# Performance work log

Hardware: AMD Instinct MI355X
Metric: run time of the kernel (lower is better)

Reference implementation:

```python
import math
import jax, jax.numpy as jnp
from jax import lax
import numpy as np

SPARSITY = 0.05
EMBEDDING_SIZE = 2048
BATCH = 32768


def setup_inputs() -> dict:
    key = jax.random.key(0)
    k0, k1, k2 = jax.random.split(key, 3)
    x = jax.random.normal(k0, (BATCH, 28, 28), dtype=jnp.float32)
    # conv: out=5, in=1, k=3, no bias (kaiming-ish scale)
    conv_w = jax.random.normal(k1, (5, 1, 3, 3), dtype=jnp.float32) * (1.0 / math.sqrt(9))
    bn_gamma = jnp.ones((5,), jnp.float32)
    bn_beta = jnp.zeros((5,), jnp.float32)
    bn_mean = jnp.zeros((5,), jnp.float32)
    bn_var = jnp.ones((5,), jnp.float32)
    # fc: [EMBEDDING_SIZE, 320], no bias
    fc_w = jax.random.normal(k2, (EMBEDDING_SIZE, 5 * 8 * 8), dtype=jnp.float32) * (1.0 / math.sqrt(320))
    return {"x": x, "conv_w": conv_w, "bn_gamma": bn_gamma, "bn_beta": bn_beta,
            "bn_mean": bn_mean, "bn_var": bn_var, "fc_w": fc_w}


def _kwta(z):
    # k-winners-take-all: top k_active entries per row -> 1, rest -> 0.
    k_active = math.ceil(SPARSITY * z.shape[1])
    topv, _ = lax.top_k(z, k_active)          # [B, k]
    thr = topv[:, -1:]                         # kth largest per row
    binary = (z >= thr).astype(z.dtype)
    # straight-through: forward = binary, backward = identity
    return z + lax.stop_gradient(binary - z)


def reference(x, conv_w, bn_gamma, bn_beta, bn_mean, bn_var, fc_w):
    h = x[:, None, :, :]  # [B,1,28,28]
    h = lax.conv_general_dilated(h, conv_w, window_strides=(1, 1), padding="VALID",
                                 dimension_numbers=("NCHW", "OIHW", "NCHW"))  # [B,5,26,26]
    inv_std = bn_gamma / jnp.sqrt(bn_var + 1e-5)
    h = (h - bn_mean[None, :, None, None]) * inv_std[None, :, None, None] + bn_beta[None, :, None, None]
    h = jnp.maximum(h, 0.0)
    # max_pool2d(kernel=3, stride=3), floor mode -> [B,5,8,8]
    h = lax.reduce_window(h, -jnp.inf, lax.max, (1, 1, 3, 3), (1, 1, 3, 3), "VALID")
    h = h.reshape(h.shape[0], -1)              # [B,320]
    z = h @ fc_w.T                             # [B,EMBEDDING_SIZE]
    return _kwta(z)
```

## Files before the change

### kernel.cpp

```cpp
#include <hip/hip_runtime.h>
#include <math.h>

#define BATCH 32768
#define EMB   2048
#define KDIM  320
#define KACT  103

#define BM 16
#define GTHREADS 512

#define CIMG 16

__global__ __launch_bounds__(256) void transpose_w_kernel(const float* __restrict__ W,
                                                          float* __restrict__ WT) {
  __shared__ float tile[32][33];
  const int k0 = blockIdx.x * 32;
  const int n0 = blockIdx.y * 32;
  const int tx = threadIdx.x;
  const int ty = threadIdx.y;
  for (int i = ty; i < 32; i += 8)
    tile[i][tx] = W[(size_t)(n0 + i) * KDIM + k0 + tx];
  __syncthreads();
  for (int i = ty; i < 32; i += 8)
    WT[(size_t)(k0 + i) * EMB + n0 + tx] = tile[tx][i];
}

__global__ __launch_bounds__(512) void conv_pool_kernel(const float* __restrict__ x,
                                                        const float* __restrict__ cw,
                                                        const float* __restrict__ gamma,
                                                        const float* __restrict__ beta,
                                                        const float* __restrict__ mean,
                                                        const float* __restrict__ var,
                                                        float* __restrict__ Ht) {
#pragma clang fp contract(off)
  __shared__ float xs[CIMG * 784];
  __shared__ float hs[KDIM * 17];
  __shared__ float wv[45];
  __shared__ float inv_s[5], mu_s[5], be_s[5];
  const int t  = threadIdx.x;
  const int b0 = blockIdx.x * CIMG;

  {
    const float4* src = (const float4*)(x + (size_t)b0 * 784);
    float4* dst = (float4*)xs;
    for (int i = t; i < CIMG * 196; i += 512) dst[i] = src[i];
  }
  if (t < 45) wv[t] = cw[t];
  if (t < 5) {
    inv_s[t] = gamma[t] / sqrtf(var[t] + 1e-5f);
    mu_s[t] = mean[t];
    be_s[t] = beta[t];
  }
  __syncthreads();

  const int i0   = t >> 6;
  const int lane = t & 63;
  const int py = lane >> 3;
  const int px = lane & 7;

  for (int ii = 0; ii < 2; ++ii) {
    const int img = i0 * 2 + ii;
    const float* xb = xs + img * 784;

    float xr[5][5];
#pragma unroll
    for (int i = 0; i < 5; ++i)
#pragma unroll
      for (int j = 0; j < 5; ++j)
        xr[i][j] = xb[(3 * py + i) * 28 + 3 * px + j];

#pragma unroll
    for (int c = 0; c < 5; ++c) {
      float wr[9];
#pragma unroll
      for (int i = 0; i < 9; ++i) wr[i] = wv[c * 9 + i];
      const float inv = inv_s[c], mu = mu_s[c], be = be_s[c];
      float mx = -__builtin_huge_valf();
#pragma unroll
      for (int ry = 0; ry < 3; ++ry)
#pragma unroll
        for (int rx = 0; rx < 3; ++rx) {
          float s = 0.0f;
#pragma unroll
          for (int di = 0; di < 3; ++di)
#pragma unroll
            for (int dj = 0; dj < 3; ++dj)
              s = __builtin_fmaf(xr[ry + di][rx + dj], wr[di * 3 + dj], s);
          float t1 = s - mu;
          float t2 = t1 * inv;
          float t3 = t2 + be;
          mx = fmaxf(mx, t3);
        }
      hs[(c * 64 + lane) * 17 + img] = fmaxf(mx, 0.0f);
    }
  }
  __syncthreads();

  for (int idx = t; idx < KDIM * CIMG; idx += 512) {
    const int k = idx >> 4;
    const int img = idx & 15;
    Ht[(size_t)k * BATCH + b0 + img] = hs[k * 17 + img];
  }
}

__global__ __launch_bounds__(GTHREADS) void gemm_topk_kernel(const float* __restrict__ Ht,
                                                             const float* __restrict__ WT,
                                                             float* __restrict__ out) {
  __shared__ unsigned histo[BM * 256];
  __shared__ unsigned prefix_s[BM];
  __shared__ unsigned rank_s[BM];

  const int t    = threadIdx.x;
  const int lane = t & 63;
  const int w    = t >> 6;
  const int m0   = blockIdx.x * BM;
  const int nt   = t * 4;

  if (t < BM) { prefix_s[t] = 0u; rank_s[t] = KACT; }

  float acc[BM][4];
#pragma unroll
  for (int m = 0; m < BM; ++m)
#pragma unroll
    for (int j = 0; j < 4; ++j) acc[m][j] = 0.0f;

  const float* Ap = Ht + m0;
  const float* wp = WT + nt;
  float4 nb0 = *(const float4*)(wp + 0 * EMB);
  float4 nb1 = *(const float4*)(wp + 1 * EMB);
  float4 nb2 = *(const float4*)(wp + 2 * EMB);
  float4 nb3 = *(const float4*)(wp + 3 * EMB);

  for (int k4 = 0; k4 < KDIM / 4; ++k4) {
    const float4 b0 = nb0, b1 = nb1, b2 = nb2, b3 = nb3;
    if (k4 + 1 < KDIM / 4) {
      const float* wn = wp + (size_t)(k4 + 1) * 4 * EMB;
      nb0 = *(const float4*)(wn + 0 * EMB);
      nb1 = *(const float4*)(wn + 1 * EMB);
      nb2 = *(const float4*)(wn + 2 * EMB);
      nb3 = *(const float4*)(wn + 3 * EMB);
    }
#pragma unroll
    for (int kk = 0; kk < 4; ++kk) {
      const float* ak = Ap + (size_t)(4 * k4 + kk) * BATCH;
      float av[BM];
#pragma unroll
      for (int m = 0; m < BM; ++m) av[m] = ak[m];
      const float4 bb = (kk == 0) ? b0 : (kk == 1) ? b1 : (kk == 2) ? b2 : b3;
#pragma unroll
      for (int m = 0; m < BM; ++m) {
        acc[m][0] = __builtin_fmaf(av[m], bb.x, acc[m][0]);
        acc[m][1] = __builtin_fmaf(av[m], bb.y, acc[m][1]);
        acc[m][2] = __builtin_fmaf(av[m], bb.z, acc[m][2]);
        acc[m][3] = __builtin_fmaf(av[m], bb.w, acc[m][3]);
      }
    }
  }
  __syncthreads();

  for (int pass = 0; pass < 4; ++pass) {
    const int shift = 24 - pass * 8;
    for (int i = t; i < BM * 256; i += GTHREADS) histo[i] = 0u;
    unsigned pref[BM];
#pragma unroll
    for (int m = 0; m < BM; ++m) pref[m] = prefix_s[m];
    __syncthreads();
#pragma unroll
    for (int m = 0; m < BM; ++m) {
#pragma unroll
      for (int j = 0; j < 4; ++j) {
        unsigned u = __float_as_uint(acc[m][j]);
        u = (u & 0x80000000u) ? ~u : (u | 0x80000000u);
        const bool in = (pass == 0) || ((u >> (shift + 8)) == pref[m]);
        if (in) atomicAdd(&histo[m * 256 + ((u >> shift) & 255u)], 1u);
      }
    }
    __syncthreads();
    for (int rr = 0; rr < 2; ++rr) {
      const int m = w * 2 + rr;
      const unsigned rank = rank_s[m];
      const uint4 c = *(const uint4*)(histo + m * 256 + lane * 4);
      const unsigned s = c.x + c.y + c.z + c.w;
      unsigned suf = s;
#pragma unroll
      for (int off = 1; off < 64; off <<= 1) {
        const unsigned o = __shfl_down(suf, off);
        if (lane + off < 64) suf += o;
      }
      const unsigned above = suf - s;
      if (above < rank && rank <= suf) {
        unsigned bin, newr;
        if (above + c.w >= rank)                    { bin = lane * 4 + 3; newr = rank - above; }
        else if (above + c.w + c.z >= rank)         { bin = lane * 4 + 2; newr = rank - above - c.w; }
        else if (above + c.w + c.z + c.y >= rank)   { bin = lane * 4 + 1; newr = rank - above - c.w - c.z; }
        else                                        { bin = lane * 4 + 0; newr = rank - above - c.w - c.z - c.y; }
        prefix_s[m] = (prefix_s[m] << 8) | bin;
        rank_s[m] = newr;
      }
    }
    __syncthreads();
  }

  unsigned thr[BM];
#pragma unroll
  for (int m = 0; m < BM; ++m) thr[m] = prefix_s[m];

#pragma unroll
  for (int m = 0; m < BM; ++m) {
    float4 o;
    float* op = (float*)&o;
#pragma unroll
    for (int j = 0; j < 4; ++j) {
      unsigned u = __float_as_uint(acc[m][j]);
      u = (u & 0x80000000u) ? ~u : (u | 0x80000000u);
      op[j] = (u >= thr[m]) ? 1.0f : 0.0f;
    }
    *(float4*)(out + (size_t)(m0 + m) * EMB + nt) = o;
  }
}

extern "C" void kernel_launch(void* const* d_in, const int* in_sizes, int n_in,
                              void* d_out, int out_size, void* d_ws, size_t ws_size,
                              hipStream_t stream) {
  const float* x      = (const float*)d_in[0];
  const float* conv_w = (const float*)d_in[1];
  const float* gamma  = (const float*)d_in[2];
  const float* beta   = (const float*)d_in[3];
  const float* mean   = (const float*)d_in[4];
  const float* var    = (const float*)d_in[5];
  const float* fc_w   = (const float*)d_in[6];
  float* out = (float*)d_out;

  float* Ht = (float*)d_ws;
  float* WT = (float*)d_ws + (size_t)KDIM * BATCH;

  transpose_w_kernel<<<dim3(KDIM / 32, EMB / 32), dim3(32, 8), 0, stream>>>(fc_w, WT);
  conv_pool_kernel<<<BATCH / CIMG, 512, 0, stream>>>(x, conv_w, gamma, beta, mean, var, Ht);
  gemm_topk_kernel<<<BATCH / BM, GTHREADS, 0, stream>>>(Ht, WT, out);
}
```

Before: 854.4 us.

## Store pooled features block-contiguously, prefetch A rows, pad histogram stride

The conv kernel now writes each 16-image block's 320x16 features as one contiguous chunk instead of strided columns across the batch, so both the conv store and the GEMM A loads become contiguous 64-byte runs. The GEMM register-prefetches the next k row of A while computing the current one to hide load latency. The per-row histogram stride is padded from 256 to 260 to reduce LDS bank conflicts on atomics. This costs extra registers for the prefetch buffers, which may lower occupancy.

```diff
diff --git a/kernel.cpp b/kernel.cpp
--- a/kernel.cpp
+++ b/kernel.cpp
@@ -10,6 +10,8 @@
 #define GTHREADS 512
 
 #define CIMG 16
+
+#define HSTRIDE 260
 
 __global__ __launch_bounds__(256) void transpose_w_kernel(const float* __restrict__ W,
                                                           float* __restrict__ WT) {
@@ -96,17 +98,18 @@
   }
   __syncthreads();
 
-  for (int idx = t; idx < KDIM * CIMG; idx += 512) {
-    const int k = idx >> 4;
-    const int img = idx & 15;
-    Ht[(size_t)k * BATCH + b0 + img] = hs[k * 17 + img];
+  float* dst = Ht + (size_t)blockIdx.x * (KDIM * CIMG);
+  for (int i = t; i < KDIM * CIMG; i += 512) {
+    const int k = i >> 4;
+    const int img = i & 15;
+    dst[i] = hs[k * 17 + img];
   }
 }
 
 __global__ __launch_bounds__(GTHREADS) void gemm_topk_kernel(const float* __restrict__ Ht,
                                                              const float* __restrict__ WT,
                                                              float* __restrict__ out) {
-  __shared__ unsigned histo[BM * 256];
+  __shared__ unsigned histo[BM * HSTRIDE];
   __shared__ unsigned prefix_s[BM];
   __shared__ unsigned rank_s[BM];
 
@@ -124,8 +127,13 @@
 #pragma unroll
     for (int j = 0; j < 4; ++j) acc[m][j] = 0.0f;
 
-  const float* Ap = Ht + m0;
+  const float* Ap = Ht + (size_t)blockIdx.x * (KDIM * BM);
   const float* wp = WT + nt;
+
+  float a_cur[BM], a_nxt[BM];
+#pragma unroll
+  for (int m = 0; m < BM; ++m) a_cur[m] = Ap[m];
+
   float4 nb0 = *(const float4*)(wp + 0 * EMB);
   float4 nb1 = *(const float4*)(wp + 1 * EMB);
   float4 nb2 = *(const float4*)(wp + 2 * EMB);
@@ -142,25 +150,29 @@
     }
 #pragma unroll
     for (int kk = 0; kk < 4; ++kk) {
-      const float* ak = Ap + (size_t)(4 * k4 + kk) * BATCH;
-      float av[BM];
-#pragma unroll
-      for (int m = 0; m < BM; ++m) av[m] = ak[m];
+      const int k = 4 * k4 + kk;
+      if (k + 1 < KDIM) {
+        const float* an = Ap + (size_t)(k + 1) * BM;
+#pragma unroll
+        for (int m = 0; m < BM; ++m) a_nxt[m] = an[m];
+      }
       const float4 bb = (kk == 0) ? b0 : (kk == 1) ? b1 : (kk == 2) ? b2 : b3;
 #pragma unroll
       for (int m = 0; m < BM; ++m) {
-        acc[m][0] = __builtin_fmaf(av[m], bb.x, acc[m][0]);
-        acc[m][1] = __builtin_fmaf(av[m], bb.y, acc[m][1]);
-        acc[m][2] = __builtin_fmaf(av[m], bb.z, acc[m][2]);
-        acc[m][3] = __builtin_fmaf(av[m], bb.w, acc[m][3]);
-      }
+        acc[m][0] = __builtin_fmaf(a_cur[m], bb.x, acc[m][0]);
+        acc[m][1] = __builtin_fmaf(a_cur[m], bb.y, acc[m][1]);
+        acc[m][2] = __builtin_fmaf(a_cur[m], bb.z, acc[m][2]);
+        acc[m][3] = __builtin_fmaf(a_cur[m], bb.w, acc[m][3]);
+      }
+#pragma unroll
+      for (int m = 0; m < BM; ++m) a_cur[m] = a_nxt[m];
     }
   }
   __syncthreads();
 
   for (int pass = 0; pass < 4; ++pass) {
     const int shift = 24 - pass * 8;
-    for (int i = t; i < BM * 256; i += GTHREADS) histo[i] = 0u;
+    for (int i = t; i < BM * HSTRIDE; i += GTHREADS) histo[i] = 0u;
     unsigned pref[BM];
 #pragma unroll
     for (int m = 0; m < BM; ++m) pref[m] = prefix_s[m];
@@ -172,14 +184,14 @@
         unsigned u = __float_as_uint(acc[m][j]);
         u = (u & 0x80000000u) ? ~u : (u | 0x80000000u);
         const bool in = (pass == 0) || ((u >> (shift + 8)) == pref[m]);
-        if (in) atomicAdd(&histo[m * 256 + ((u >> shift) & 255u)], 1u);
+        if (in) atomicAdd(&histo[m * HSTRIDE + ((u >> shift) & 255u)], 1u);
       }
     }
     __syncthreads();
     for (int rr = 0; rr < 2; ++rr) {
       const int m = w * 2 + rr;
       const unsigned rank = rank_s[m];
-      const uint4 c = *(const uint4*)(histo + m * 256 + lane * 4);
+      const uint4 c = *(const uint4*)(histo + m * HSTRIDE + lane * 4);
       const unsigned s = c.x + c.y + c.z + c.w;
       unsigned suf = s;
 #pragma unroll
```

Measured after the change: 1.177 ms. 1.38x slower.

## Block-contiguous H layout and replicated padded histograms for top-k selection

Applied to the files above, without the earlier changes.

The conv kernel now writes pooled features as contiguous per-block tiles of 320x16 instead of a k-major BATCH-strided layout. The GEMM then reads its A operand from one contiguous 20KB chunk rather than 320 rows spaced far apart. The radix-select histogram is split into two copies, one per half of the waves, padded to a stride of 260 to reduce atomic contention and bank conflicts. The sortable-key conversion is also hoisted out of the pass loop, at the cost of more registers and extra LDS clearing.

```diff
diff --git a/kernel.cpp b/kernel.cpp
--- a/kernel.cpp
+++ b/kernel.cpp
@@ -10,6 +10,9 @@
 #define GTHREADS 512
 
 #define CIMG 16
+
+#define HSTRIDE 260
+#define HCOPY 2
 
 __global__ __launch_bounds__(256) void transpose_w_kernel(const float* __restrict__ W,
                                                           float* __restrict__ WT) {
@@ -96,17 +99,18 @@
   }
   __syncthreads();
 
-  for (int idx = t; idx < KDIM * CIMG; idx += 512) {
-    const int k = idx >> 4;
-    const int img = idx & 15;
-    Ht[(size_t)k * BATCH + b0 + img] = hs[k * 17 + img];
+  float* dst = Ht + (size_t)blockIdx.x * (KDIM * CIMG);
+  for (int i = t; i < KDIM * CIMG; i += 512) {
+    const int k = i >> 4;
+    const int img = i & 15;
+    dst[i] = hs[k * 17 + img];
   }
 }
 
 __global__ __launch_bounds__(GTHREADS) void gemm_topk_kernel(const float* __restrict__ Ht,
                                                              const float* __restrict__ WT,
                                                              float* __restrict__ out) {
-  __shared__ unsigned histo[BM * 256];
+  __shared__ unsigned histo[HCOPY * BM * HSTRIDE];
   __shared__ unsigned prefix_s[BM];
   __shared__ unsigned rank_s[BM];
 
@@ -124,7 +128,7 @@
 #pragma unroll
     for (int j = 0; j < 4; ++j) acc[m][j] = 0.0f;
 
-  const float* Ap = Ht + m0;
+  const float* Ap = Ht + (size_t)blockIdx.x * (KDIM * BM);
   const float* wp = WT + nt;
   float4 nb0 = *(const float4*)(wp + 0 * EMB);
   float4 nb1 = *(const float4*)(wp + 1 * EMB);
@@ -142,7 +146,7 @@
     }
 #pragma unroll
     for (int kk = 0; kk < 4; ++kk) {
-      const float* ak = Ap + (size_t)(4 * k4 + kk) * BATCH;
+      const float* ak = Ap + (size_t)(4 * k4 + kk) * BM;
       float av[BM];
 #pragma unroll
       for (int m = 0; m < BM; ++m) av[m] = ak[m];
@@ -156,11 +160,23 @@
       }
     }
   }
+
+  unsigned ua[BM][4];
+#pragma unroll
+  for (int m = 0; m < BM; ++m)
+#pragma unroll
+    for (int j = 0; j < 4; ++j) {
+      unsigned u = __float_as_uint(acc[m][j]);
+      ua[m][j] = (u & 0x80000000u) ? ~u : (u | 0x80000000u);
+    }
+
+  unsigned* hc = histo + (w >> 2) * (BM * HSTRIDE);
+
   __syncthreads();
 
   for (int pass = 0; pass < 4; ++pass) {
     const int shift = 24 - pass * 8;
-    for (int i = t; i < BM * 256; i += GTHREADS) histo[i] = 0u;
+    for (int i = t; i < HCOPY * BM * HSTRIDE; i += GTHREADS) histo[i] = 0u;
     unsigned pref[BM];
 #pragma unroll
     for (int m = 0; m < BM; ++m) pref[m] = prefix_s[m];
@@ -169,17 +185,19 @@
     for (int m = 0; m < BM; ++m) {
 #pragma unroll
       for (int j = 0; j < 4; ++j) {
-        unsigned u = __float_as_uint(acc[m][j]);
-        u = (u & 0x80000000u) ? ~u : (u | 0x80000000u);
+        const unsigned u = ua[m][j];
         const bool in = (pass == 0) || ((u >> (shift + 8)) == pref[m]);
-        if (in) atomicAdd(&histo[m * 256 + ((u >> shift) & 255u)], 1u);
+        if (in) atomicAdd(&hc[m * HSTRIDE + ((u >> shift) & 255u)], 1u);
       }
     }
     __syncthreads();
     for (int rr = 0; rr < 2; ++rr) {
       const int m = w * 2 + rr;
       const unsigned rank = rank_s[m];
-      const uint4 c = *(const uint4*)(histo + m * 256 + lane * 4);
+      const uint4 c0 = *(const uint4*)(histo + m * HSTRIDE + lane * 4);
+      const uint4 c1 = *(const uint4*)(histo + BM * HSTRIDE + m * HSTRIDE + lane * 4);
+      uint4 c;
+      c.x = c0.x + c1.x; c.y = c0.y + c1.y; c.z = c0.z + c1.z; c.w = c0.w + c1.w;
       const unsigned s = c.x + c.y + c.z + c.w;
       unsigned suf = s;
 #pragma unroll
@@ -210,11 +228,8 @@
     float4 o;
     float* op = (float*)&o;
 #pragma unroll
-    for (int j = 0; j < 4; ++j) {
-      unsigned u = __float_as_uint(acc[m][j]);
-      u = (u & 0x80000000u) ? ~u : (u | 0x80000000u);
-      op[j] = (u >= thr[m]) ? 1.0f : 0.0f;
-    }
+    for (int j = 0; j < 4; ++j)
+      op[j] = (ua[m][j] >= thr[m]) ? 1.0f : 0.0f;
     *(float4*)(out + (size_t)(m0 + m) * EMB + nt) = o;
   }
 }
```

After: 1.212 ms. 1.42x slower.
